# Kernel tuning notes

Hardware: AMD Instinct MI355X
Metric: run time of the kernel (lower is better)

Reference implementation:

```python
import jax, jax.numpy as jnp
import numpy as np

NHEAD = 8
MAX_RADIUS = 16
NEG_INF = float('-inf')


def setup_inputs() -> dict:
    key = jax.random.key(0)
    ks = jax.random.split(key, 6)
    B, T, D = 4, 2048, 512
    s = 1.0 / np.sqrt(D)
    return {
        'x': jax.random.normal(ks[0], (B, T, D), dtype=jnp.float32),
        'radius': jax.random.normal(ks[1], (NHEAD,), dtype=jnp.float32),
        'in_proj_weight': jax.random.normal(ks[2], (3 * D, D), dtype=jnp.float32) * s,
        'in_proj_bias': jax.random.normal(ks[3], (3 * D,), dtype=jnp.float32) * 0.02,
        'out_proj_weight': jax.random.normal(ks[4], (D, D), dtype=jnp.float32) * s,
        'out_proj_bias': jax.random.normal(ks[5], (D,), dtype=jnp.float32) * 0.02,
    }


def reference(x, radius, in_proj_weight, in_proj_bias, out_proj_weight, out_proj_bias):
    B, T, D = x.shape
    H = NHEAD
    hd = D // H
    scale = 1.0 / jnp.sqrt(jnp.asarray(hd, dtype=x.dtype))

    # fused QKV projection: [B,T,3D]
    qkv = x @ in_proj_weight.T + in_proj_bias
    q, k, v = jnp.split(qkv, 3, axis=-1)
    q = q.reshape(B, T, H, hd)
    k = k.reshape(B, T, H, hd)
    v = v.reshape(B, T, H, hd)

    # scores [B,H,T,T]
    scores = jnp.einsum('bqhd,bkhd->bhqk', q, k) * scale

    # per-head learned radius band mask
    r = jnp.clip(jax.nn.sigmoid(radius) * MAX_RADIUS, 1.0)  # [H]
    idx = jnp.arange(T)
    rel = jnp.abs(idx[None, :] - idx[:, None]).astype(x.dtype)  # [T,T]
    band = rel[None, :, :] <= r[:, None, None]  # [H,T,T]
    scores = jnp.where(band[None], scores, NEG_INF)

    attn = jax.nn.softmax(scores, axis=-1)
    out = jnp.einsum('bhqk,bkhd->bqhd', attn, v).reshape(B, T, D)
    return out @ out_proj_weight.T + out_proj_bias
```

## Files before the change

### kernel.cpp

```cpp
#include <hip/hip_runtime.h>
#include <hip/hip_bf16.h>
#include <cstdint>

#define T_LEN 2048
#define B_SZ 4
#define D_MOD 512
#define N_HEAD 8
#define HDIM 64
#define QKV_N 1536
#define M_ROWS 8192

typedef uint32_t u32;
typedef uint16_t u16;
typedef __attribute__((ext_vector_type(8))) __bf16 bf16x8;
typedef __attribute__((ext_vector_type(4))) float f32x4;

__device__ __forceinline__ u16 f2bf(float f) {
    u32 u = __builtin_bit_cast(u32, f);
    u32 r = (u + 0x7FFFu + ((u >> 16) & 1u)) >> 16;
    return (u16)r;
}
__device__ __forceinline__ float bf2f(u16 h) {
    u32 u = ((u32)h) << 16;
    return __builtin_bit_cast(float, u);
}

__global__ void cast3_kernel(const float* __restrict__ a, int na,
                             const float* __restrict__ b, int nb,
                             const float* __restrict__ c,
                             u16* __restrict__ oa, u16* __restrict__ ob, u16* __restrict__ oc) {
    int i8 = (blockIdx.x * blockDim.x + threadIdx.x) * 8;
    const float* src; u16* dst; int off;
    if (i8 < na)           { src = a; dst = oa; off = i8; }
    else if (i8 < na + nb) { src = b; dst = ob; off = i8 - na; }
    else                   { src = c; dst = oc; off = i8 - na - nb; }
    const float4* p = (const float4*)(src + off);
    float4 x = p[0], y = p[1];
    u32 r0 = (u32)f2bf(x.x) | ((u32)f2bf(x.y) << 16);
    u32 r1 = (u32)f2bf(x.z) | ((u32)f2bf(x.w) << 16);
    u32 r2 = (u32)f2bf(y.x) | ((u32)f2bf(y.y) << 16);
    u32 r3 = (u32)f2bf(y.z) | ((u32)f2bf(y.w) << 16);
    *(uint4*)(dst + off) = make_uint4(r0, r1, r2, r3);
}

#define BK 64

template <bool OUT_BF16, int BMt, int BNt>
__global__ __launch_bounds__(256, 2)
void gemm_bt(const u16* __restrict__ A, const u16* __restrict__ B,
             const float* __restrict__ bias, void* __restrict__ C,
             int M, int N, int K)
{
    constexpr int WM = BMt / 2;
    constexpr int WN = BNt / 2;
    constexpr int MI = WM / 16;
    constexpr int NI = WN / 16;
    __shared__ alignas(16) u16 lda[BMt * BK];
    __shared__ alignas(16) u16 ldb[BNt * BK];
    const int tid  = threadIdx.x;
    const int wave = tid >> 6;
    const int lane = tid & 63;
    const int bn = blockIdx.x, bm = blockIdx.y;
    const int wm = wave >> 1, wn = wave & 1;

    f32x4 acc[MI][NI] = {};

    const int srow8 = lane >> 3;
    const int sg    = (lane & 7) ^ srow8;
    const long a_base = (long)bm * BMt;
    const long b_base = (long)bn * BNt;

    const int fr = lane & 15;
    const int fq = lane >> 4;
    int a_off[MI], b_off[NI];
#pragma unroll
    for (int i = 0; i < MI; ++i) {
        int ra = wm * WM + i * 16 + fr;
        a_off[i] = ra * BK + ((fq ^ (ra & 7)) * 8);
    }
#pragma unroll
    for (int i = 0; i < NI; ++i) {
        int rb = wn * WN + i * 16 + fr;
        b_off[i] = rb * BK + ((fq ^ (rb & 7)) * 8);
    }

    for (int kk = 0; kk < K; kk += BK) {
#pragma unroll
        for (int j = 0; j < BMt / 32; ++j) {
            int r = wave * (BMt / 4) + j * 8 + srow8;
            const u16* ga = A + (a_base + r) * (long)K + kk + sg * 8;
            __builtin_amdgcn_global_load_lds(
                (const __attribute__((address_space(1))) void*)ga,
                (__attribute__((address_space(3))) void*)&lda[(wave * (BMt / 4) + j * 8) * BK],
                16, 0, 0);
        }
#pragma unroll
        for (int j = 0; j < BNt / 32; ++j) {
            int r = wave * (BNt / 4) + j * 8 + srow8;
            const u16* gb = B + (b_base + r) * (long)K + kk + sg * 8;
            __builtin_amdgcn_global_load_lds(
                (const __attribute__((address_space(1))) void*)gb,
                (__attribute__((address_space(3))) void*)&ldb[(wave * (BNt / 4) + j * 8) * BK],
                16, 0, 0);
        }
        __syncthreads();
#pragma unroll
        for (int kh = 0; kh < 2; ++kh) {
            bf16x8 af[MI], bfr[NI];
#pragma unroll
            for (int i = 0; i < MI; ++i) af[i]  = *(const bf16x8*)&lda[a_off[i] ^ (kh << 5)];
#pragma unroll
            for (int i = 0; i < NI; ++i) bfr[i] = *(const bf16x8*)&ldb[b_off[i] ^ (kh << 5)];
#pragma unroll
            for (int mi = 0; mi < MI; ++mi)
#pragma unroll
                for (int ni = 0; ni < NI; ++ni)
                    acc[mi][ni] = __builtin_amdgcn_mfma_f32_16x16x32_bf16(
                        af[mi], bfr[ni], acc[mi][ni], 0, 0, 0);
        }
        __syncthreads();
    }

    const long row0 = a_base + wm * WM;
    const long col0 = b_base + wn * WN;
#pragma unroll
    for (int mi = 0; mi < MI; ++mi) {
#pragma unroll
        for (int ni = 0; ni < NI; ++ni) {
            long col = col0 + ni * 16 + fr;
            float bv = bias[col];
            long rowb = row0 + mi * 16 + fq * 4;
#pragma unroll
            for (int rr = 0; rr < 4; ++rr) {
                float v = acc[mi][ni][rr] + bv;
                long idx = (rowb + rr) * (long)N + col;
                if (OUT_BF16) ((u16*)C)[idx] = f2bf(v);
                else          ((float*)C)[idx] = v;
            }
        }
    }
}

#define AQ 128
#define AW 16
#define AROWS (AQ + 2 * AW)
#define ASTR 70

__device__ __forceinline__ void unpack16(const u32* __restrict__ src, float* __restrict__ dst) {
#pragma unroll
    for (int dd = 0; dd < 8; ++dd) {
        u32 wv = src[dd];
        dst[2 * dd]     = bf2f((u16)(wv & 0xffffu));
        dst[2 * dd + 1] = bf2f((u16)(wv >> 16));
    }
}

__global__ __launch_bounds__(256)
void attn_kernel(const u16* __restrict__ qkv, const float* __restrict__ radius,
                 u16* __restrict__ out)
{
    __shared__ u16 ks[AROWS * ASTR];
    __shared__ u16 vs[AROWS * ASTR];

    const int tid = threadIdx.x;
    const int bid = blockIdx.x;
    const int qc = bid & 15;
    const int h  = (bid >> 4) & 7;
    const int b  = bid >> 7;
    const int q0 = qc * AQ;

    float rad = radius[h];
    float r = fmaxf(16.0f / (1.0f + __expf(-rad)), 1.0f);
    const int w = (int)floorf(r);

    for (int cid = tid; cid < AROWS * 4; cid += 256) {
        int row = cid >> 2;
        int ch  = cid & 3;
        int t = min(max(q0 - AW + row, 0), T_LEN - 1);
        const u16* gk = qkv + ((long)(b * T_LEN + t)) * QKV_N + D_MOD + h * HDIM + ch * 16;
        const u16* gv = gk + D_MOD;
        uint4 k0 = *(const uint4*)gk, k1 = *(const uint4*)(gk + 8);
        uint4 v0 = *(const uint4*)gv, v1 = *(const uint4*)(gv + 8);
        u32* kd = (u32*)&ks[row * ASTR + ch * 18];
        u32* vd = (u32*)&vs[row * ASTR + ch * 18];
        kd[0] = k0.x; kd[1] = k0.y; kd[2] = k0.z; kd[3] = k0.w;
        kd[4] = k1.x; kd[5] = k1.y; kd[6] = k1.z; kd[7] = k1.w;
        vd[0] = v0.x; vd[1] = v0.y; vd[2] = v0.z; vd[3] = v0.w;
        vd[4] = v1.x; vd[5] = v1.y; vd[6] = v1.z; vd[7] = v1.w;
    }

    const int p = tid >> 2;
    const int g = tid & 3;
    const int qA = q0 + 2 * p;
    const long rowA = (long)(b * T_LEN + qA);
    const long rowB = rowA + 1;

    float qregA[16], qregB[16];
    {
        const u16* gq = qkv + rowA * QKV_N + h * HDIM + g * 16;
        u32 wa[8], wb[8];
        uint4 t0 = *(const uint4*)gq,              t1 = *(const uint4*)(gq + 8);
        uint4 t2 = *(const uint4*)(gq + QKV_N),    t3 = *(const uint4*)(gq + QKV_N + 8);
        wa[0]=t0.x; wa[1]=t0.y; wa[2]=t0.z; wa[3]=t0.w; wa[4]=t1.x; wa[5]=t1.y; wa[6]=t1.z; wa[7]=t1.w;
        wb[0]=t2.x; wb[1]=t2.y; wb[2]=t2.z; wb[3]=t2.w; wb[4]=t3.x; wb[5]=t3.y; wb[6]=t3.z; wb[7]=t3.w;
#pragma unroll
        for (int j = 0; j < 8; ++j) {
            qregA[2 * j]     = bf2f((u16)(wa[j] & 0xffffu)) * 0.125f;
            qregA[2 * j + 1] = bf2f((u16)(wa[j] >> 16))     * 0.125f;
            qregB[2 * j]     = bf2f((u16)(wb[j] & 0xffffu)) * 0.125f;
            qregB[2 * j + 1] = bf2f((u16)(wb[j] >> 16))     * 0.125f;
        }
    }
    __syncthreads();

    float mA = -1e30f, lA = 0.0f, mB = -1e30f, lB = 0.0f;
    float accA[16], accB[16];
#pragma unroll
    for (int d = 0; d < 16; ++d) { accA[d] = 0.0f; accB[d] = 0.0f; }

    const int imax = 2 * w + 1;
    for (int i = 0; i <= imax; ++i) {
        int jrow = 2 * p - w + i;
        int j = q0 + jrow;
        int row = jrow + AW;
        float kf[16];
        unpack16((const u32*)&ks[row * ASTR + g * 18], kf);
        float sA = 0.0f, sB = 0.0f;
#pragma unroll
        for (int d = 0; d < 16; ++d) { sA += qregA[d] * kf[d]; sB += qregB[d] * kf[d]; }
        sA += __shfl_xor(sA, 1); sA += __shfl_xor(sA, 2);
        sB += __shfl_xor(sB, 1); sB += __shfl_xor(sB, 2);
        bool inb = ((unsigned)j) < (unsigned)T_LEN;
        bool vA = inb && (i < imax);
        bool vB = inb && (i > 0);
        float mnA = fmaxf(mA, vA ? sA : -1e30f);
        float scA = __expf(mA - mnA);
        float pA  = vA ? __expf(sA - mnA) : 0.0f;
        mA = mnA; lA = lA * scA + pA;
        float mnB = fmaxf(mB, vB ? sB : -1e30f);
        float scB = __expf(mB - mnB);
        float pB  = vB ? __expf(sB - mnB) : 0.0f;
        mB = mnB; lB = lB * scB + pB;
        float vf[16];
        unpack16((const u32*)&vs[row * ASTR + g * 18], vf);
#pragma unroll
        for (int d = 0; d < 16; ++d) {
            accA[d] = accA[d] * scA + pA * vf[d];
            accB[d] = accB[d] * scB + pB * vf[d];
        }
    }

    float invA = 1.0f / lA;
    float invB = 1.0f / lB;
    u32 oA[8], oB[8];
#pragma unroll
    for (int j2 = 0; j2 < 8; ++j2) {
        oA[j2] = (u32)f2bf(accA[2 * j2] * invA) | ((u32)f2bf(accA[2 * j2 + 1] * invA) << 16);
        oB[j2] = (u32)f2bf(accB[2 * j2] * invB) | ((u32)f2bf(accB[2 * j2 + 1] * invB) << 16);
    }
    u16* poA = out + rowA * D_MOD + h * HDIM + g * 16;
    u16* poB = out + rowB * D_MOD + h * HDIM + g * 16;
    *(uint4*)poA       = make_uint4(oA[0], oA[1], oA[2], oA[3]);
    *(uint4*)(poA + 8) = make_uint4(oA[4], oA[5], oA[6], oA[7]);
    *(uint4*)poB       = make_uint4(oB[0], oB[1], oB[2], oB[3]);
    *(uint4*)(poB + 8) = make_uint4(oB[4], oB[5], oB[6], oB[7]);
}

extern "C" void kernel_launch(void* const* d_in, const int* in_sizes, int n_in,
                              void* d_out, int out_size, void* d_ws, size_t ws_size,
                              hipStream_t stream)
{
    (void)in_sizes; (void)n_in; (void)out_size; (void)ws_size;
    const float* x      = (const float*)d_in[0];
    const float* radius = (const float*)d_in[1];
    const float* w_in   = (const float*)d_in[2];
    const float* b_in   = (const float*)d_in[3];
    const float* w_out  = (const float*)d_in[4];
    const float* b_out  = (const float*)d_in[5];
    float* outp = (float*)d_out;

    char* ws = (char*)d_ws;
    u16* x_bf    = (u16*)ws;  ws += (size_t)M_ROWS * D_MOD * 2;
    u16* win_bf  = (u16*)ws;  ws += (size_t)QKV_N * D_MOD * 2;
    u16* wout_bf = (u16*)ws;  ws += (size_t)D_MOD * D_MOD * 2;
    u16* qkv_bf  = (u16*)ws;  ws += (size_t)M_ROWS * QKV_N * 2;
    u16* attn_bf = (u16*)ws;

    const int na = M_ROWS * D_MOD;
    const int nb = QKV_N * D_MOD;
    const int nc = D_MOD * D_MOD;
    cast3_kernel<<<(na + nb + nc) / 2048, 256, 0, stream>>>(
        x, na, w_in, nb, w_out, x_bf, win_bf, wout_bf);

    gemm_bt<true, 128, 192><<<dim3(QKV_N / 192, M_ROWS / 128), 256, 0, stream>>>(
        x_bf, win_bf, b_in, qkv_bf, M_ROWS, QKV_N, D_MOD);
    attn_kernel<<<B_SZ * N_HEAD * (T_LEN / AQ), 256, 0, stream>>>(qkv_bf, radius, attn_bf);
    gemm_bt<false, 64, 128><<<dim3(D_MOD / 128, M_ROWS / 64), 256, 0, stream>>>(
        attn_bf, wout_bf, b_out, outp, M_ROWS, D_MOD, D_MOD);
}
```

Measured before the change: 127.3 us.

## Double GEMM K-tile to 128 and vectorize epilogue via swapped MFMA operands

Raises the GEMM K-tile from 64 to 128 and reworks the LDS XOR swizzle and load mapping for 16 chunks per row. This halves the number of barrier pairs per K loop. The MFMA operands are swapped so each lane holds four consecutive columns, which lets the epilogue do vectorized float4 bias loads and 8- or 16-byte stores instead of scalar strided stores. It doubles LDS per block, which may lower occupancy under launch_bounds(256,2).

New measurement: 132.2 us. 3.8% more time.

```diff
diff --git a/kernel.cpp b/kernel.cpp
--- a/kernel.cpp
+++ b/kernel.cpp
@@ -43,7 +43,7 @@
     *(uint4*)(dst + off) = make_uint4(r0, r1, r2, r3);
 }
 
-#define BK 64
+#define BK 128
 
 template <bool OUT_BF16, int BMt, int BNt>
 __global__ __launch_bounds__(256, 2)
@@ -65,8 +65,8 @@
 
     f32x4 acc[MI][NI] = {};
 
-    const int srow8 = lane >> 3;
-    const int sg    = (lane & 7) ^ srow8;
+    const int srow4 = lane >> 4;
+    const int l15   = lane & 15;
     const long a_base = (long)bm * BMt;
     const long b_base = (long)bn * BNt;
 
@@ -76,36 +76,40 @@
 #pragma unroll
     for (int i = 0; i < MI; ++i) {
         int ra = wm * WM + i * 16 + fr;
-        a_off[i] = ra * BK + ((fq ^ (ra & 7)) * 8);
+        a_off[i] = ra * BK + ((fq ^ (ra & 15)) * 8);
     }
 #pragma unroll
     for (int i = 0; i < NI; ++i) {
         int rb = wn * WN + i * 16 + fr;
-        b_off[i] = rb * BK + ((fq ^ (rb & 7)) * 8);
+        b_off[i] = rb * BK + ((fq ^ (rb & 15)) * 8);
     }
 
     for (int kk = 0; kk < K; kk += BK) {
 #pragma unroll
-        for (int j = 0; j < BMt / 32; ++j) {
-            int r = wave * (BMt / 4) + j * 8 + srow8;
+        for (int j = 0; j < BMt / 16; ++j) {
+            int rloc = j * 4 + srow4;
+            int r = wave * (BMt / 4) + rloc;
+            int sg = l15 ^ (rloc & 15);
             const u16* ga = A + (a_base + r) * (long)K + kk + sg * 8;
             __builtin_amdgcn_global_load_lds(
                 (const __attribute__((address_space(1))) void*)ga,
-                (__attribute__((address_space(3))) void*)&lda[(wave * (BMt / 4) + j * 8) * BK],
+                (__attribute__((address_space(3))) void*)&lda[(wave * (BMt / 4) + j * 4) * BK],
                 16, 0, 0);
         }
 #pragma unroll
-        for (int j = 0; j < BNt / 32; ++j) {
-            int r = wave * (BNt / 4) + j * 8 + srow8;
+        for (int j = 0; j < BNt / 16; ++j) {
+            int rloc = j * 4 + srow4;
+            int r = wave * (BNt / 4) + rloc;
+            int sg = l15 ^ (rloc & 15);
             const u16* gb = B + (b_base + r) * (long)K + kk + sg * 8;
             __builtin_amdgcn_global_load_lds(
                 (const __attribute__((address_space(1))) void*)gb,
-                (__attribute__((address_space(3))) void*)&ldb[(wave * (BNt / 4) + j * 8) * BK],
+                (__attribute__((address_space(3))) void*)&ldb[(wave * (BNt / 4) + j * 4) * BK],
                 16, 0, 0);
         }
         __syncthreads();
 #pragma unroll
-        for (int kh = 0; kh < 2; ++kh) {
+        for (int kh = 0; kh < 4; ++kh) {
             bf16x8 af[MI], bfr[NI];
 #pragma unroll
             for (int i = 0; i < MI; ++i) af[i]  = *(const bf16x8*)&lda[a_off[i] ^ (kh << 5)];
@@ -116,7 +120,7 @@
 #pragma unroll
                 for (int ni = 0; ni < NI; ++ni)
                     acc[mi][ni] = __builtin_amdgcn_mfma_f32_16x16x32_bf16(
-                        af[mi], bfr[ni], acc[mi][ni], 0, 0, 0);
+                        bfr[ni], af[mi], acc[mi][ni], 0, 0, 0);
         }
         __syncthreads();
     }
@@ -125,17 +129,22 @@
     const long col0 = b_base + wn * WN;
 #pragma unroll
     for (int mi = 0; mi < MI; ++mi) {
+        long row = row0 + mi * 16 + fr;
 #pragma unroll
         for (int ni = 0; ni < NI; ++ni) {
-            long col = col0 + ni * 16 + fr;
-            float bv = bias[col];
-            long rowb = row0 + mi * 16 + fq * 4;
-#pragma unroll
-            for (int rr = 0; rr < 4; ++rr) {
-                float v = acc[mi][ni][rr] + bv;
-                long idx = (rowb + rr) * (long)N + col;
-                if (OUT_BF16) ((u16*)C)[idx] = f2bf(v);
-                else          ((float*)C)[idx] = v;
+            long col = col0 + ni * 16 + fq * 4;
+            float4 bv = *(const float4*)&bias[col];
+            float v0 = acc[mi][ni][0] + bv.x;
+            float v1 = acc[mi][ni][1] + bv.y;
+            float v2 = acc[mi][ni][2] + bv.z;
+            float v3 = acc[mi][ni][3] + bv.w;
+            long idx = row * (long)N + col;
+            if (OUT_BF16) {
+                u32 lo = (u32)f2bf(v0) | ((u32)f2bf(v1) << 16);
+                u32 hi = (u32)f2bf(v2) | ((u32)f2bf(v3) << 16);
+                *(uint2*)((u16*)C + idx) = make_uint2(lo, hi);
+            } else {
+                *(float4*)((float*)C + idx) = make_float4(v0, v1, v2, v3);
             }
         }
     }
```
